# Performance work log

Measured on AMD Instinct MI355X. Metric: run time of the kernel, lower is better.

Reference implementation:

```python
import jax, jax.numpy as jnp
import numpy as np
from jax import lax

S_DET, S_ANG = 725, 360   # detector bins, projection angles
OUT = 512                 # reconstructed image side
NNZ = 8388608             # nonzeros in sparse backprojection matrix AT
BATCH = 4
BN_EPS = 1e-3             # keras BatchNormalization default epsilon


def _ramp_filter():
    # w_bfunction(pi, linspace(-362, 362, 725))
    s = np.linspace(-np.floor(S_DET / 2), S_DET - np.floor(S_DET / 2) - 1, S_DET)
    v = np.pi * s
    u = np.empty_like(v)
    z = v == 0
    u[z] = 0.5
    nz = ~z
    u[nz] = (np.cos(v[nz]) - 1.0) / v[nz] ** 2 + np.sin(v[nz]) / v[nz]
    return (u * np.pi ** 2 / (4.0 * np.pi ** 2)).astype(np.float32)


def setup_inputs() -> dict:
    key = jax.random.key(0)
    ks = jax.random.split(key, 24)
    p = 0.05
    inp = {
        'inputs': jax.random.normal(ks[0], (BATCH, S_DET, S_ANG, 1), jnp.float32),
        'w_sin1': jax.random.normal(ks[1], (5, 5, 1, 64), jnp.float32) * p,
        'b_sin1': jnp.zeros((64,), jnp.float32),
        'w_sin_mid': jax.random.normal(ks[2], (4, 5, 5, 64, 64), jnp.float32) * p,
        'sin_gamma': jnp.ones((4, 64), jnp.float32),
        'sin_beta': jnp.zeros((4, 64), jnp.float32),
        'sin_mean': jax.random.normal(ks[3], (4, 64), jnp.float32) * 0.1,
        'sin_var': jax.random.uniform(ks[4], (4, 64), jnp.float32, 0.5, 1.5),
        'w_sin6': jax.random.normal(ks[5], (5, 5, 64, 1), jnp.float32) * p,
        'b_sin6': jnp.zeros((1,), jnp.float32),
        'w_ct1': jax.random.normal(ks[6], (5, 5, 1, 64), jnp.float32) * p,
        'b_ct1': jnp.zeros((64,), jnp.float32),
        'w_ct_mid': jax.random.normal(ks[7], (5, 5, 5, 64, 64), jnp.float32) * p,
        'ct_gamma': jnp.ones((5, 64), jnp.float32),
        'ct_beta': jnp.zeros((5, 64), jnp.float32),
        'ct_mean': jax.random.normal(ks[8], (5, 64), jnp.float32) * 0.1,
        'ct_var': jax.random.uniform(ks[9], (5, 64), jnp.float32, 0.5, 1.5),
        'w_ct6': jax.random.normal(ks[10], (5, 5, 64, 1), jnp.float32) * p,
        'b_ct6': jnp.zeros((1,), jnp.float32),
        'w_b': jnp.asarray(_ramp_filter()),
        'at_vals': jax.random.uniform(ks[11], (NNZ,), jnp.float32) * 1e-3,
        'at_rows': jnp.sort(jax.random.randint(ks[12], (NNZ,), 0, OUT * OUT, jnp.int32)),
        'at_cols': jax.random.randint(ks[13], (NNZ,), 0, S_DET * S_ANG, jnp.int32),
    }
    return inp


def _conv2d(x, w, b=None):
    y = lax.conv_general_dilated(x, w, (1, 1), 'SAME',
                                 dimension_numbers=('NHWC', 'HWIO', 'NHWC'))
    return y if b is None else y + b


def _bn(x, g, b, m, v):
    return (x - m) * (g * lax.rsqrt(v + BN_EPS)) + b


def _decode(sin_fan, w_b, at_vals, at_rows, at_cols):
    B = sin_fan.shape[0]
    sf = jnp.transpose(sin_fan, (0, 2, 1, 3))          # [B, 360, 725, 1]
    x = sf.reshape(-1, S_DET, 1)                       # [B*360, 725, 1]
    k = w_b.reshape(S_DET, 1, 1)
    f = lax.conv_general_dilated(x, k, (1,), 'SAME',
                                 dimension_numbers=('NWC', 'WIO', 'NWC'))
    f2 = f.reshape(B, -1).T                            # [261000, B]
    # sparse AT @ f2 via gather + segment_sum
    contrib = at_vals[:, None] * f2[at_cols]           # [nnz, B]
    rf = jax.ops.segment_sum(contrib, at_rows, num_segments=OUT * OUT)
    return 4.0 * rf.T.reshape(B, OUT, OUT, 1)


def reference(inputs, w_sin1, b_sin1, w_sin_mid, sin_gamma, sin_beta, sin_mean,
              sin_var, w_sin6, b_sin6, w_ct1, b_ct1, w_ct_mid, ct_gamma,
              ct_beta, ct_mean, ct_var, w_ct6, b_ct6, w_b, at_vals,
              at_rows, at_cols):
    # --- sinogram domain residual CNN ---
    de = jax.nn.relu(_conv2d(inputs, w_sin1, b_sin1))
    pp = de
    for i in range(4):  # M1 residual blocks
        de = jax.nn.relu(_bn(_conv2d(de, w_sin_mid[i]), sin_gamma[i],
                             sin_beta[i], sin_mean[i], sin_var[i]))
        pp = de + pp
    de_sin = _conv2d(pp / 4.0, w_sin6, b_sin6) + inputs
    # --- filtered backprojection ---
    fbp = _decode(de_sin, w_b, at_vals, at_rows, at_cols)
    # --- image domain residual CNN ---
    out = jax.nn.relu(_conv2d(fbp, w_ct1, b_ct1))
    qq = out
    for i in range(5):  # M2 residual blocks
        out = jax.nn.relu(_bn(_conv2d(out, w_ct_mid[i]), ct_gamma[i],
                              ct_beta[i], ct_mean[i], ct_var[i]))
        qq = qq + out
    outputs = _conv2d(qq / 5.0, w_ct6, b_ct6) + fbp
    return (de_sin, outputs, fbp)
```

## Files before the change

### kernel.cpp

```cpp
#include <hip/hip_runtime.h>
#include <stdint.h>

#define S_DET 725
#define S_ANG 360
#define OUTD  512
#define NB    4

typedef float    float4v __attribute__((ext_vector_type(4)));
typedef int      int4v   __attribute__((ext_vector_type(4)));
typedef _Float16 half8   __attribute__((ext_vector_type(8)));
typedef _Float16 half4   __attribute__((ext_vector_type(4)));
typedef _Float16 half2v  __attribute__((ext_vector_type(2)));

#define GAS __attribute__((address_space(1)))
#define LAS __attribute__((address_space(3)))

__device__ __forceinline__ void async16(const void* src, void* lds) {
  __builtin_amdgcn_global_load_lds((const GAS void*)(uintptr_t)src,
                                   (LAS void*)(uint32_t)(uintptr_t)lds, 16, 0, 0);
}

__global__ __launch_bounds__(256)
void prep_weights(const float* __restrict__ wsin, const float* __restrict__ sg,
                  const float* __restrict__ sb,  const float* __restrict__ sm,
                  const float* __restrict__ sv,
                  const float* __restrict__ wct, const float* __restrict__ cg,
                  const float* __restrict__ cbt, const float* __restrict__ cm,
                  const float* __restrict__ cv,
                  const float* __restrict__ wsin6, const float* __restrict__ wct6,
                  const float* __restrict__ wsin1, const float* __restrict__ wct1,
                  _Float16* __restrict__ wout, float* __restrict__ bout,
                  _Float16* __restrict__ w6out, _Float16* __restrict__ w1fout)
{
  int id = blockIdx.x * 256 + threadIdx.x;
  if (id < 9 * 102400) {
    int l   = id / 102400;
    int rem = id - l * 102400;
    int t = rem >> 12;
    int kn = rem & 4095;
    int k = kn >> 6, n = kn & 63;
    const float *w, *g, *b, *m, *v;
    if (l < 4) { w = wsin + l*102400; g = sg + l*64; b = sb + l*64; m = sm + l*64; v = sv + l*64; }
    else { int li = l - 4; w = wct + li*102400; g = cg + li*64; b = cbt + li*64; m = cm + li*64; v = cv + li*64; }
    float s = g[n] * rsqrtf(v[n] + 1e-3f);
    float val = w[rem] * s;
    int slot = (k >> 3) ^ (n & 7);
    wout[(size_t)l*102400 + t*4096 + n*64 + slot*8 + (k & 7)] = (_Float16)val;
    if (rem < 64)
      bout[l*64 + rem] = b[rem] - m[rem] * s;
  } else {
    int r = id - 9 * 102400;
    if (r < 3200) {
      w6out[r] = (_Float16)(r < 1600 ? wsin6[r] : wct6[r - 1600]);
    } else if (r < 3200 + 4096) {
      int q = r - 3200;
      int layer = q >> 11;
      int idx = q & 2047;
      int ci = idx >> 9, ln = (idx >> 3) & 63, e = idx & 7;
      int ch = ci * 16 + (ln & 15);
      int k = (ln >> 4) * 8 + e;
      float val = 0.f;
      if (k < 25) val = (layer ? wct1 : wsin1)[k * 64 + ch];
      w1fout[q] = (_Float16)val;
    }
  }
}

template <int IMG>
__global__ __launch_bounds__(256)
void conv1_mfma(const float* __restrict__ src, _Float16* __restrict__ dst,
                const _Float16* __restrict__ w1f, const float* __restrict__ b1,
                int H, int W, int b0)
{
  __shared__ __align__(16) float rawt[400];
  __shared__ __align__(16) char imc[256 * 80];
  const int tid = threadIdx.x;
  const int wv = tid >> 6, ln = tid & 63;
  const int bz = blockIdx.z, gb = b0 + bz;
  const int y0 = blockIdx.y * 16, x0 = blockIdx.x * 16;
  for (int i = tid; i < 400; i += 256) {
    int iy = i / 20, ix = i - iy * 20;
    int y = y0 - 2 + iy, x = x0 - 2 + ix;
    float v = 0.f;
    if (y >= 0 && y < H && x >= 0 && x < W) {
      if (IMG) v = 4.f * src[(size_t)(y * W + x) * 4 + gb];
      else     v = src[((size_t)gb * H + y) * W + x];
    }
    rawt[i] = v;
  }
  __syncthreads();
  {
    const int ty = tid >> 4, tx = tid & 15;
    _Float16 row[32];
    int dy = 0, dx = 0;
#pragma unroll
    for (int t = 0; t < 25; ++t) {
      row[t] = (_Float16)rawt[(ty + dy) * 20 + tx + dx];
      if (++dx == 5) { dx = 0; ++dy; }
    }
#pragma unroll
    for (int t = 25; t < 32; ++t) row[t] = (_Float16)0.f;
    char* dp = imc + tid * 80;
#pragma unroll
    for (int j = 0; j < 4; ++j)
      *(half8*)(dp + j * 16) = *(const half8*)((const char*)row + j * 16);
  }
  __syncthreads();

  half8 wf[4];
#pragma unroll
  for (int ci = 0; ci < 4; ++ci) wf[ci] = ((const half8*)w1f)[ci * 64 + ln];

  float4v acc[4][4];
#pragma unroll
  for (int pi = 0; pi < 4; ++pi)
#pragma unroll
    for (int ci = 0; ci < 4; ++ci) acc[pi][ci] = (float4v){0.f, 0.f, 0.f, 0.f};

#pragma unroll
  for (int pi = 0; pi < 4; ++pi) {
    const int px = (wv * 4 + pi) * 16 + (ln & 15);
    half8 af = *(const half8*)(imc + px * 80 + ((ln >> 4) << 4));
#pragma unroll
    for (int ci = 0; ci < 4; ++ci)
      acc[pi][ci] = __builtin_amdgcn_mfma_f32_16x16x32_f16(wf[ci], af, acc[pi][ci], 0, 0, 0);
  }

  const int tx = ln & 15;
  const int x = x0 + tx;
#pragma unroll
  for (int pi = 0; pi < 4; ++pi) {
    const int y = y0 + wv * 4 + pi;
    if (y < H && x < W) {
      _Float16* dp = dst + ((size_t)(bz * H + y) * W + x) * 64;
#pragma unroll
      for (int ci = 0; ci < 4; ++ci) {
        const int cbase = ci * 16 + (ln >> 4) * 4;
        const float4v bv = *(const float4v*)(b1 + cbase);
        half4 h;
#pragma unroll
        for (int r = 0; r < 4; ++r) {
          float v = acc[pi][ci][r] + bv[r];
          v = v > 0.f ? v : 0.f;
          h[r] = (_Float16)v;
        }
        *(half4*)(dp + cbase) = h;
      }
    }
  }
}

__global__ __launch_bounds__(256, 2)
void mid_conv(const _Float16* __restrict__ src, _Float16* __restrict__ dst,
              float* __restrict__ accum,
              const _Float16* __restrict__ wt, const _Float16* __restrict__ w6g,
              const float* __restrict__ bias, const char* __restrict__ zbuf,
              int H, int W, int b0)
{
  __shared__ __align__(16) char smem[51200 + 2 * 8192];
  char* const atile = smem;
  char* const wbuf  = smem + 51200;
  const int tid = threadIdx.x;
  const int wv = tid >> 6, ln = tid & 63;
  const int bz = blockIdx.z, gb = b0 + bz;
  const int y0 = blockIdx.y * 16, x0 = blockIdx.x * 16;

  for (int inst = wv; inst < 50; inst += 4) {
    const int slot = inst * 64 + ln;
    const int p = slot >> 3, gp = slot & 7;
    const int g = gp ^ (p & 7);
    const int iy = p / 20, ix = p - iy * 20;
    const int y = y0 - 2 + iy, x = x0 - 2 + ix;
    const char* sp = (y >= 0 && y < H && x >= 0 && x < W)
        ? (const char*)(src + ((size_t)(bz * H + y) * W + x) * 64) + g * 16
        : zbuf + g * 16;
    async16(sp, atile + inst * 1024);
  }
#pragma unroll
  for (int j = 0; j < 2; ++j) {
    const int inst = wv * 2 + j;
    async16((const char*)wt + inst * 1024 + ln * 16, wbuf + inst * 1024);
  }
  __syncthreads();

  float4v acc[4][4];
  float4v acc6[4];
#pragma unroll
  for (int pi = 0; pi < 4; ++pi) {
    acc6[pi] = (float4v){0.f, 0.f, 0.f, 0.f};
#pragma unroll
    for (int ci = 0; ci < 4; ++ci) acc[pi][ci] = (float4v){0.f, 0.f, 0.f, 0.f};
  }

  int dy = 0, dx = 0;
  for (int t = 0; t < 25; ++t) {
    if (t < 24) {
      char* wdst = wbuf + ((t + 1) & 1) * 8192;
#pragma unroll
      for (int j = 0; j < 2; ++j) {
        const int inst = wv * 2 + j;
        async16((const char*)wt + (t + 1) * 8192 + inst * 1024 + ln * 16,
                wdst + inst * 1024);
      }
    }
    const char* wb = wbuf + (t & 1) * 8192;
#pragma unroll
    for (int kc = 0; kc < 2; ++kc) {
      const int g0 = kc * 4 + (ln >> 4);
      half8 wf[4], af[4];
      half8 wf6 = {(_Float16)0, (_Float16)0, (_Float16)0, (_Float16)0,
                   (_Float16)0, (_Float16)0, (_Float16)0, (_Float16)0};
#pragma unroll
      for (int ci = 0; ci < 4; ++ci) {
        const int ch = ci * 16 + (ln & 15);
        wf[ci] = *(const half8*)(wb + ch * 128 + ((g0 ^ (ch & 7)) << 4));
      }
      if ((ln & 15) == 0)
        wf6 = *(const half8*)(w6g + t * 64 + kc * 32 + ((ln >> 4) << 3));
#pragma unroll
      for (int pi = 0; pi < 4; ++pi) {
        const int p = (wv * 4 + pi + dy) * 20 + (ln & 15) + dx;
        af[pi] = *(const half8*)(atile + p * 128 + ((g0 ^ (p & 7)) << 4));
      }
#pragma unroll
      for (int pi = 0; pi < 4; ++pi) {
#pragma unroll
        for (int ci = 0; ci < 4; ++ci)
          acc[pi][ci] = __builtin_amdgcn_mfma_f32_16x16x32_f16(
              wf[ci], af[pi], acc[pi][ci], 0, 0, 0);
        acc6[pi] = __builtin_amdgcn_mfma_f32_16x16x32_f16(
            wf6, af[pi], acc6[pi], 0, 0, 0);
      }
    }
    if (++dx == 5) { dx = 0; ++dy; }
    __syncthreads();
  }

  const int tx = ln & 15;
  const int x = x0 + tx;
#pragma unroll
  for (int pi = 0; pi < 4; ++pi) {
    const int y = y0 + wv * 4 + pi;
    if (y < H && x < W) {
      _Float16* dp = dst + ((size_t)(bz * H + y) * W + x) * 64;
#pragma unroll
      for (int ci = 0; ci < 4; ++ci) {
        const int cbase = ci * 16 + (ln >> 4) * 4;
        const float4v bv = *(const float4v*)(bias + cbase);
        half4 h;
#pragma unroll
        for (int r = 0; r < 4; ++r) {
          float v = acc[pi][ci][r] + bv[r];
          v = v > 0.f ? v : 0.f;
          h[r] = (_Float16)v;
        }
        *(half4*)(dp + cbase) = h;
      }
    }
  }
  if (ln < 16) {
#pragma unroll
    for (int pi = 0; pi < 4; ++pi) {
      const int y = y0 + wv * 4 + pi, x2 = x0 + ln;
      if (y < H && x2 < W)
        accum[((size_t)gb * H + y) * W + x2] += acc6[pi][0];
    }
  }
}

__global__ __launch_bounds__(256, 3)
void fc_mfma(const _Float16* __restrict__ src, float* __restrict__ accum,
             const _Float16* __restrict__ w6g, const char* __restrict__ zbuf,
             int H, int W, int b0)
{
  __shared__ __align__(16) char atile[51200];
  const int tid = threadIdx.x;
  const int wv = tid >> 6, ln = tid & 63;
  const int bz = blockIdx.z, gb = b0 + bz;
  const int y0 = blockIdx.y * 16, x0 = blockIdx.x * 16;
  for (int inst = wv; inst < 50; inst += 4) {
    const int slot = inst * 64 + ln;
    const int p = slot >> 3, gp = slot & 7;
    const int g = gp ^ (p & 7);
    const int iy = p / 20, ix = p - iy * 20;
    const int y = y0 - 2 + iy, x = x0 - 2 + ix;
    const char* sp = (y >= 0 && y < H && x >= 0 && x < W)
        ? (const char*)(src + ((size_t)(bz * H + y) * W + x) * 64) + g * 16
        : zbuf + g * 16;
    async16(sp, atile + inst * 1024);
  }
  __syncthreads();

  float4v acc6[4];
#pragma unroll
  for (int pi = 0; pi < 4; ++pi) acc6[pi] = (float4v){0.f, 0.f, 0.f, 0.f};

  int dy = 0, dx = 0;
  for (int t = 0; t < 25; ++t) {
#pragma unroll
    for (int kc = 0; kc < 2; ++kc) {
      const int g0 = kc * 4 + (ln >> 4);
      half8 wf6 = {(_Float16)0, (_Float16)0, (_Float16)0, (_Float16)0,
                   (_Float16)0, (_Float16)0, (_Float16)0, (_Float16)0};
      if ((ln & 15) == 0)
        wf6 = *(const half8*)(w6g + t * 64 + kc * 32 + ((ln >> 4) << 3));
#pragma unroll
      for (int pi = 0; pi < 4; ++pi) {
        const int p = (wv * 4 + pi + dy) * 20 + (ln & 15) + dx;
        half8 af = *(const half8*)(atile + p * 128 + ((g0 ^ (p & 7)) << 4));
        acc6[pi] = __builtin_amdgcn_mfma_f32_16x16x32_f16(wf6, af, acc6[pi], 0, 0, 0);
      }
    }
    if (++dx == 5) { dx = 0; ++dy; }
  }
  if (ln < 16) {
#pragma unroll
    for (int pi = 0; pi < 4; ++pi) {
      const int y = y0 + wv * 4 + pi, x2 = x0 + ln;
      if (y < H && x2 < W)
        accum[((size_t)gb * H + y) * W + x2] += acc6[pi][0];
    }
  }
}

__global__ __launch_bounds__(256)
void write_desin(const float* __restrict__ accf, const float* __restrict__ inputs,
                 const float* __restrict__ b6, float* __restrict__ out)
{
  int id = blockIdx.x * 256 + threadIdx.x;
  if (id < NB * S_DET * S_ANG) out[id] = accf[id] * 0.25f + b6[0] + inputs[id];
}

__global__ __launch_bounds__(128)
void ramp_filter(const float* __restrict__ desin, const float* __restrict__ wb,
                 _Float16* __restrict__ f2h)
{
  __shared__ float col[1472];
  __shared__ float wl[725];
  const int blk = blockIdx.x;
  const int b = blk / 360, a = blk - b * 360;
  const int tid = threadIdx.x;
  for (int i = tid; i < 1472; i += 128) col[i] = 0.f;
  for (int i = tid; i < 725; i += 128) wl[i] = wb[i];
  __syncthreads();
  for (int i = tid; i < 725; i += 128) col[368 + i] = desin[(b * 725 + i) * 360 + a];
  __syncthreads();
  const int s0 = tid * 6;
  if (s0 < 725) {
    float o0 = 0, o1 = 0, o2 = 0, o3 = 0, o4 = 0, o5 = 0;
    const float* cb = col + 6 + s0;
    float r0 = cb[0], r1 = cb[1], r2 = cb[2], r3 = cb[3], r4 = cb[4], r5 = cb[5];
    for (int t = 0; t < 725; ++t) {
      float w = wl[t];
      o0 += r0 * w; o1 += r1 * w; o2 += r2 * w;
      o3 += r3 * w; o4 += r4 * w; o5 += r5 * w;
      r0 = r1; r1 = r2; r2 = r3; r3 = r4; r4 = r5; r5 = cb[t + 6];
    }
    float o[6] = { o0, o1, o2, o3, o4, o5 };
#pragma unroll
    for (int j = 0; j < 6; ++j)
      if (s0 + j < 725) f2h[((size_t)a * 725 + s0 + j) * 4 + b] = (_Float16)o[j];
  }
}

__global__ __launch_bounds__(256)
void backproj(const float* __restrict__ vals, const int* __restrict__ rows,
              const int* __restrict__ cols, const _Float16* __restrict__ f2h,
              float* __restrict__ rf)
{
  const int tid = blockIdx.x * 256 + threadIdx.x;
  const size_t i0 = (size_t)tid * 64;
  const int4v* rp = (const int4v*)(rows + i0);
  const int4v* cp = (const int4v*)(cols + i0);
  const float4v* vp = (const float4v*)(vals + i0);
  float a0 = 0, a1 = 0, a2 = 0, a3 = 0;
  int4v r0v = __builtin_nontemporal_load(rp);
  int cur = r0v[0];
  bool first = true;
#pragma unroll 4
  for (int q = 0; q < 16; ++q) {
    int4v r4 = (q == 0) ? r0v : __builtin_nontemporal_load(rp + q);
    int4v c4 = __builtin_nontemporal_load(cp + q);
    float4v v4 = __builtin_nontemporal_load(vp + q);
#pragma unroll
    for (int u = 0; u < 4; ++u) {
      int r = r4[u]; int c = c4[u]; float v = v4[u];
      if (r != cur) {
        float* p = rf + (size_t)cur * 4;
        if (first) {
          atomicAdd(p + 0, a0); atomicAdd(p + 1, a1);
          atomicAdd(p + 2, a2); atomicAdd(p + 3, a3);
          first = false;
        } else {
          p[0] = a0; p[1] = a1; p[2] = a2; p[3] = a3;
        }
        a0 = a1 = a2 = a3 = 0; cur = r;
      }
      const half4 f = *(const half4*)(f2h + (size_t)c * 4);
      a0 += v * (float)f[0]; a1 += v * (float)f[1];
      a2 += v * (float)f[2]; a3 += v * (float)f[3];
    }
  }
  float* p = rf + (size_t)cur * 4;
  atomicAdd(p + 0, a0); atomicAdd(p + 1, a1);
  atomicAdd(p + 2, a2); atomicAdd(p + 3, a3);
}

__global__ __launch_bounds__(256)
void write_fbp(const float* __restrict__ rf, float* __restrict__ out)
{
  int id = blockIdx.x * 256 + threadIdx.x;
  int b = id >> 18, p = id & 262143;
  out[id] = 4.f * rf[(size_t)p * 4 + b];
}

__global__ __launch_bounds__(256)
void write_outputs(const float* __restrict__ accf, const float* __restrict__ rf,
                   const float* __restrict__ b6, float* __restrict__ out)
{
  int id = blockIdx.x * 256 + threadIdx.x;
  int b = id >> 18, p = id & 262143;
  out[id] = accf[id] * 0.2f + b6[0] + 4.f * rf[(size_t)p * 4 + b];
}

extern "C" void kernel_launch(void* const* d_in, const int* in_sizes, int n_in,
                              void* d_out, int out_size, void* d_ws, size_t ws_size,
                              hipStream_t stream)
{
  (void)in_sizes; (void)n_in; (void)out_size;
  const float* inputs   = (const float*)d_in[0];
  const float* w_sin1   = (const float*)d_in[1];
  const float* b_sin1   = (const float*)d_in[2];
  const float* w_sin_mid= (const float*)d_in[3];
  const float* sin_gamma= (const float*)d_in[4];
  const float* sin_beta = (const float*)d_in[5];
  const float* sin_mean = (const float*)d_in[6];
  const float* sin_var  = (const float*)d_in[7];
  const float* w_sin6   = (const float*)d_in[8];
  const float* b_sin6   = (const float*)d_in[9];
  const float* w_ct1    = (const float*)d_in[10];
  const float* b_ct1    = (const float*)d_in[11];
  const float* w_ct_mid = (const float*)d_in[12];
  const float* ct_gamma = (const float*)d_in[13];
  const float* ct_beta  = (const float*)d_in[14];
  const float* ct_mean  = (const float*)d_in[15];
  const float* ct_var   = (const float*)d_in[16];
  const float* w_ct6    = (const float*)d_in[17];
  const float* b_ct6    = (const float*)d_in[18];
  const float* w_b      = (const float*)d_in[19];
  const float* at_vals  = (const float*)d_in[20];
  const int*   at_rows  = (const int*)d_in[21];
  const int*   at_cols  = (const int*)d_in[22];
  float* out = (float*)d_out;

  const size_t base = (size_t)11 << 20;
  const size_t act_per_batch = (size_t)2 * 262144 * 128;
  int nbat = 1;
  if (ws_size >= base + 4 * act_per_batch) nbat = 4;
  else if (ws_size >= base + 2 * act_per_batch) nbat = 2;
  const int npass = 4 / nbat;

  char* ws = (char*)d_ws;
  size_t off = 0;
  auto alloc = [&](size_t bytes) {
    char* p = ws + off;
    off = (off + bytes + 255) & ~(size_t)255;
    return p;
  };
  char*     zbuf    = alloc(256);
  _Float16* wmid    = (_Float16*)alloc((size_t)9 * 102400 * 2);
  float*    biasmid = (float*)alloc(9 * 64 * 4);
  _Float16* w6s     = (_Float16*)alloc(3200 * 2);
  _Float16* w1f     = (_Float16*)alloc(4096 * 2);
  float*    rf      = (float*)alloc((size_t)262144 * 16);
  char*     shreg   = alloc((size_t)262144 * 16);
  _Float16* act_a   = (_Float16*)alloc((size_t)nbat * 262144 * 128);
  _Float16* act_b   = (_Float16*)alloc((size_t)nbat * 262144 * 128);
  _Float16* f2h    = (_Float16*)shreg;
  float*    acc_fc = (float*)shreg;

  hipMemsetAsync(zbuf, 0, 256, stream);
  hipMemsetAsync(rf, 0, (size_t)262144 * 16, stream);
  hipMemsetAsync(acc_fc, 0, (size_t)262144 * 16, stream);

  prep_weights<<<3630, 256, 0, stream>>>(w_sin_mid, sin_gamma, sin_beta, sin_mean, sin_var,
                                         w_ct_mid, ct_gamma, ct_beta, ct_mean, ct_var,
                                         w_sin6, w_ct6, w_sin1, w_ct1,
                                         wmid, biasmid, w6s, w1f);

  for (int p = 0; p < npass; ++p) {
    const int b0 = p * nbat;
    conv1_mfma<0><<<dim3(23, 46, nbat), 256, 0, stream>>>(inputs, act_a, w1f, b_sin1,
                                                          725, 360, b0);
    _Float16* cur = act_a; _Float16* nxt = act_b;
    for (int i = 0; i < 4; ++i) {
      mid_conv<<<dim3(23, 46, nbat), 256, 0, stream>>>(cur, nxt, acc_fc,
                                                       wmid + (size_t)i * 102400, w6s,
                                                       biasmid + i * 64, zbuf, 725, 360, b0);
      _Float16* t = cur; cur = nxt; nxt = t;
    }
    fc_mfma<<<dim3(23, 46, nbat), 256, 0, stream>>>(cur, acc_fc, w6s, zbuf, 725, 360, b0);
  }
  write_desin<<<4079, 256, 0, stream>>>(acc_fc, inputs, b_sin6, out);

  ramp_filter<<<1440, 128, 0, stream>>>(out, w_b, f2h);
  backproj<<<512, 256, 0, stream>>>(at_vals, at_rows, at_cols, f2h, rf);
  write_fbp<<<4096, 256, 0, stream>>>(rf, out + 2092576);

  hipMemsetAsync(acc_fc, 0, (size_t)262144 * 16, stream);
  for (int p = 0; p < npass; ++p) {
    const int b0 = p * nbat;
    conv1_mfma<1><<<dim3(32, 32, nbat), 256, 0, stream>>>(rf, act_a, w1f + 2048, b_ct1,
                                                          512, 512, b0);
    _Float16* cur = act_a; _Float16* nxt = act_b;
    for (int i = 0; i < 5; ++i) {
      mid_conv<<<dim3(32, 32, nbat), 256, 0, stream>>>(cur, nxt, acc_fc,
                                                       wmid + (size_t)(4 + i) * 102400,
                                                       w6s + 1600,
                                                       biasmid + (4 + i) * 64, zbuf,
                                                       512, 512, b0);
      _Float16* t = cur; cur = nxt; nxt = t;
    }
    fc_mfma<<<dim3(32, 32, nbat), 256, 0, stream>>>(cur, acc_fc, w6s + 1600, zbuf,
                                                    512, 512, b0);
  }
  write_outputs<<<4096, 256, 0, stream>>>(acc_fc, rf, b_ct6, out + 1044000);
}
```

Measured before the change: 2.871 ms.

## Restructure mid_conv into 512-thread 16x32 tiles with LDS-resident weights

The mid-layer conv kernel now uses 512 threads covering a 16x32 output tile and splits the 64 input channels into two halves. For each half it loads all 25 taps of weights (100 KB) plus the input halo into LDS at once, so the per-tap double-buffered weight prefetch and the barrier after every tap are gone. Weights are repacked into a new half/tap/group layout to match. Separately, backprojection work per thread is halved and the grid doubled. The cost is about 150 KB of LDS per block, which limits residency (launch bounds ask for two blocks per CU), and there is less overlap between loading and compute.

```diff
diff --git a/kernel.cpp b/kernel.cpp
--- a/kernel.cpp
+++ b/kernel.cpp
@@ -44,8 +44,8 @@
     else { int li = l - 4; w = wct + li*102400; g = cg + li*64; b = cbt + li*64; m = cm + li*64; v = cv + li*64; }
     float s = g[n] * rsqrtf(v[n] + 1e-3f);
     float val = w[rem] * s;
-    int slot = (k >> 3) ^ (n & 7);
-    wout[(size_t)l*102400 + t*4096 + n*64 + slot*8 + (k & 7)] = (_Float16)val;
+    int h = k >> 5, gc = (k >> 3) & 3, e = k & 7;
+    wout[(size_t)l*102400 + h*51200 + t*2048 + gc*512 + n*8 + e] = (_Float16)val;
     if (rem < 64)
       bout[l*64 + rem] = b[rem] - m[rem] * s;
   } else {
@@ -150,38 +150,25 @@
   }
 }
 
-__global__ __launch_bounds__(256, 2)
+__global__ __launch_bounds__(512, 2)
 void mid_conv(const _Float16* __restrict__ src, _Float16* __restrict__ dst,
               float* __restrict__ accum,
               const _Float16* __restrict__ wt, const _Float16* __restrict__ w6g,
               const float* __restrict__ bias, const char* __restrict__ zbuf,
               int H, int W, int b0)
 {
-  __shared__ __align__(16) char smem[51200 + 2 * 8192];
+  __shared__ __align__(16) char smem[46080 + 102400 + 3200 + 16];
   char* const atile = smem;
-  char* const wbuf  = smem + 51200;
+  char* const wlds  = smem + 46080;
+  _Float16* const w6l = (_Float16*)(smem + 148480);
+  char* const zsl = smem + 151680;
   const int tid = threadIdx.x;
   const int wv = tid >> 6, ln = tid & 63;
   const int bz = blockIdx.z, gb = b0 + bz;
-  const int y0 = blockIdx.y * 16, x0 = blockIdx.x * 16;
-
-  for (int inst = wv; inst < 50; inst += 4) {
-    const int slot = inst * 64 + ln;
-    const int p = slot >> 3, gp = slot & 7;
-    const int g = gp ^ (p & 7);
-    const int iy = p / 20, ix = p - iy * 20;
-    const int y = y0 - 2 + iy, x = x0 - 2 + ix;
-    const char* sp = (y >= 0 && y < H && x >= 0 && x < W)
-        ? (const char*)(src + ((size_t)(bz * H + y) * W + x) * 64) + g * 16
-        : zbuf + g * 16;
-    async16(sp, atile + inst * 1024);
-  }
-#pragma unroll
-  for (int j = 0; j < 2; ++j) {
-    const int inst = wv * 2 + j;
-    async16((const char*)wt + inst * 1024 + ln * 16, wbuf + inst * 1024);
-  }
-  __syncthreads();
+  const int y0 = blockIdx.y * 16, x0 = blockIdx.x * 32;
+
+  if (tid < 200) ((half8*)w6l)[tid] = ((const half8*)w6g)[tid];
+  if (tid < 4) ((int*)zsl)[tid] = 0;
 
   float4v acc[4][4];
   float4v acc6[4];
@@ -192,35 +179,38 @@
     for (int ci = 0; ci < 4; ++ci) acc[pi][ci] = (float4v){0.f, 0.f, 0.f, 0.f};
   }
 
-  int dy = 0, dx = 0;
-  for (int t = 0; t < 25; ++t) {
-    if (t < 24) {
-      char* wdst = wbuf + ((t + 1) & 1) * 8192;
-#pragma unroll
-      for (int j = 0; j < 2; ++j) {
-        const int inst = wv * 2 + j;
-        async16((const char*)wt + (t + 1) * 8192 + inst * 1024 + ln * 16,
-                wdst + inst * 1024);
-      }
-    }
-    const char* wb = wbuf + (t & 1) * 8192;
-#pragma unroll
-    for (int kc = 0; kc < 2; ++kc) {
-      const int g0 = kc * 4 + (ln >> 4);
-      half8 wf[4], af[4];
-      half8 wf6 = {(_Float16)0, (_Float16)0, (_Float16)0, (_Float16)0,
-                   (_Float16)0, (_Float16)0, (_Float16)0, (_Float16)0};
-#pragma unroll
-      for (int ci = 0; ci < 4; ++ci) {
-        const int ch = ci * 16 + (ln & 15);
-        wf[ci] = *(const half8*)(wb + ch * 128 + ((g0 ^ (ch & 7)) << 4));
-      }
-      if ((ln & 15) == 0)
-        wf6 = *(const half8*)(w6g + t * 64 + kc * 32 + ((ln >> 4) << 3));
+  for (int h = 0; h < 2; ++h) {
+    if (h) __syncthreads();
+    for (int inst = wv; inst < 45; inst += 8) {
+      const int s = inst * 64 + ln;
+      const int g = s / 720;
+      const int px = s - g * 720;
+      const int iy = px / 36, ix = px - iy * 36;
+      const int y = y0 - 2 + iy, x = x0 - 2 + ix;
+      const char* sp = (y >= 0 && y < H && x >= 0 && x < W)
+          ? (const char*)(src + ((size_t)(bz * H + y) * W + x) * 64) + (h * 4 + g) * 16
+          : zbuf + g * 16;
+      async16(sp, atile + inst * 1024);
+    }
+    const char* wsrc = (const char*)wt + h * 102400;
+    for (int inst = wv; inst < 100; inst += 8)
+      async16(wsrc + inst * 1024 + ln * 16, wlds + inst * 1024);
+    __syncthreads();
+
+    int dy = 0, dx = 0;
+    const int gq = ln >> 4;
+    for (int t = 0; t < 25; ++t) {
+      half8 wf[4], af[4], wf6;
+#pragma unroll
+      for (int ci = 0; ci < 4; ++ci)
+        wf[ci] = *(const half8*)(wlds + t * 4096 + gq * 1024 + (ci * 16 + (ln & 15)) * 16);
+      wf6 = *(const half8*)(((ln & 15) == 0)
+              ? (const char*)w6l + t * 128 + h * 64 + gq * 16
+              : zsl);
 #pragma unroll
       for (int pi = 0; pi < 4; ++pi) {
-        const int p = (wv * 4 + pi + dy) * 20 + (ln & 15) + dx;
-        af[pi] = *(const half8*)(atile + p * 128 + ((g0 ^ (p & 7)) << 4));
+        const int px = (wv * 2 + (pi >> 1) + dy) * 36 + (pi & 1) * 16 + (ln & 15) + dx;
+        af[pi] = *(const half8*)(atile + gq * 11520 + px * 16);
       }
 #pragma unroll
       for (int pi = 0; pi < 4; ++pi) {
@@ -231,37 +221,37 @@
         acc6[pi] = __builtin_amdgcn_mfma_f32_16x16x32_f16(
             wf6, af[pi], acc6[pi], 0, 0, 0);
       }
-    }
-    if (++dx == 5) { dx = 0; ++dy; }
-    __syncthreads();
+      if (++dx == 5) { dx = 0; ++dy; }
+    }
   }
 
   const int tx = ln & 15;
-  const int x = x0 + tx;
 #pragma unroll
   for (int pi = 0; pi < 4; ++pi) {
-    const int y = y0 + wv * 4 + pi;
+    const int y = y0 + wv * 2 + (pi >> 1);
+    const int x = x0 + (pi & 1) * 16 + tx;
     if (y < H && x < W) {
       _Float16* dp = dst + ((size_t)(bz * H + y) * W + x) * 64;
 #pragma unroll
       for (int ci = 0; ci < 4; ++ci) {
         const int cbase = ci * 16 + (ln >> 4) * 4;
         const float4v bv = *(const float4v*)(bias + cbase);
-        half4 h;
+        half4 hh;
 #pragma unroll
         for (int r = 0; r < 4; ++r) {
           float v = acc[pi][ci][r] + bv[r];
           v = v > 0.f ? v : 0.f;
-          h[r] = (_Float16)v;
+          hh[r] = (_Float16)v;
         }
-        *(half4*)(dp + cbase) = h;
+        *(half4*)(dp + cbase) = hh;
       }
     }
   }
   if (ln < 16) {
 #pragma unroll
     for (int pi = 0; pi < 4; ++pi) {
-      const int y = y0 + wv * 4 + pi, x2 = x0 + ln;
+      const int y = y0 + wv * 2 + (pi >> 1);
+      const int x2 = x0 + (pi & 1) * 16 + ln;
       if (y < H && x2 < W)
         accum[((size_t)gb * H + y) * W + x2] += acc6[pi][0];
     }
@@ -369,7 +359,7 @@
               float* __restrict__ rf)
 {
   const int tid = blockIdx.x * 256 + threadIdx.x;
-  const size_t i0 = (size_t)tid * 64;
+  const size_t i0 = (size_t)tid * 32;
   const int4v* rp = (const int4v*)(rows + i0);
   const int4v* cp = (const int4v*)(cols + i0);
   const float4v* vp = (const float4v*)(vals + i0);
@@ -378,7 +368,7 @@
   int cur = r0v[0];
   bool first = true;
 #pragma unroll 4
-  for (int q = 0; q < 16; ++q) {
+  for (int q = 0; q < 8; ++q) {
     int4v r4 = (q == 0) ? r0v : __builtin_nontemporal_load(rp + q);
     int4v c4 = __builtin_nontemporal_load(cp + q);
     float4v v4 = __builtin_nontemporal_load(vp + q);
@@ -494,7 +484,7 @@
                                                           725, 360, b0);
     _Float16* cur = act_a; _Float16* nxt = act_b;
     for (int i = 0; i < 4; ++i) {
-      mid_conv<<<dim3(23, 46, nbat), 256, 0, stream>>>(cur, nxt, acc_fc,
+      mid_conv<<<dim3(12, 46, nbat), 512, 0, stream>>>(cur, nxt, acc_fc,
                                                        wmid + (size_t)i * 102400, w6s,
                                                        biasmid + i * 64, zbuf, 725, 360, b0);
       _Float16* t = cur; cur = nxt; nxt = t;
@@ -504,7 +494,7 @@
   write_desin<<<4079, 256, 0, stream>>>(acc_fc, inputs, b_sin6, out);
 
   ramp_filter<<<1440, 128, 0, stream>>>(out, w_b, f2h);
-  backproj<<<512, 256, 0, stream>>>(at_vals, at_rows, at_cols, f2h, rf);
+  backproj<<<1024, 256, 0, stream>>>(at_vals, at_rows, at_cols, f2h, rf);
   write_fbp<<<4096, 256, 0, stream>>>(rf, out + 2092576);
 
   hipMemsetAsync(acc_fc, 0, (size_t)262144 * 16, stream);
@@ -514,7 +504,7 @@
                                                           512, 512, b0);
     _Float16* cur = act_a; _Float16* nxt = act_b;
     for (int i = 0; i < 5; ++i) {
-      mid_conv<<<dim3(32, 32, nbat), 256, 0, stream>>>(cur, nxt, acc_fc,
+      mid_conv<<<dim3(16, 32, nbat), 512, 0, stream>>>(cur, nxt, acc_fc,
                                                        wmid + (size_t)(4 + i) * 102400,
                                                        w6s + 1600,
                                                        biasmid + (4 + i) * 64, zbuf,
```

After: 3.173 ms. +10.5%, slower.
